# Performance work log

Hardware: AMD Instinct MI355X
Metric: run time of the kernel (lower is better)

The kernel has to match this reference:

```python
import jax, jax.numpy as jnp
import numpy as np


def _sdpa(q, k, v):
    # q: [B,H,Sq,D], k/v: [B,H,Sk,D]; torch F.scaled_dot_product_attention default scale
    scale = 1.0 / np.sqrt(q.shape[-1]).astype(np.float32)
    logits = jnp.einsum('bhqd,bhkd->bhqk', q, k) * scale
    w = jax.nn.softmax(logits, axis=-1)
    return jnp.einsum('bhqk,bhkd->bhqd', w, v)


def setup_inputs() -> dict:
    key = jax.random.key(0)
    ks = jax.random.split(key, 8)
    B2, S, C = 4, 1024, 1280  # full batch = [noise; ref], SDXL-like 32x32 latent
    Bh = B2 // 2
    w_init = 1.0 / np.sqrt(C).astype(np.float32)
    return {
        'hidden_states': jax.random.normal(ks[0], (B2, S, C), jnp.float32),
        'mask_ref': jax.random.uniform(ks[1], (Bh, S, 1), jnp.float32),
        'Wq': jax.random.normal(ks[2], (C, C), jnp.float32) * w_init,
        'Wk': jax.random.normal(ks[3], (C, C), jnp.float32) * w_init,
        'Wv': jax.random.normal(ks[4], (C, C), jnp.float32) * w_init,
        'Wo': jax.random.normal(ks[5], (C, C), jnp.float32) * w_init,
        'bo': jnp.zeros((C,), jnp.float32),
        'heads': 20,
    }


def reference(hidden_states, mask_ref, Wq, Wk, Wv, Wo, bo, heads):
    module_scale = 1.0  # self.scale
    B2, S, C = hidden_states.shape
    B = B2 // 2
    H = heads
    D = C // H
    noise = hidden_states[:B]
    ref = hidden_states[B:]

    # NOTE: faithful to source quirk: query uses the FULL 2B batch, then is
    # viewed as (B, 2S, H, D) -> q has query length 2S.
    query = jnp.einsum('bsc,oc->bso', hidden_states, Wq)  # [2B,S,C]
    q = query.reshape(B, 2 * S, H, D).transpose(0, 2, 1, 3)  # [B,H,2S,D]

    # background branch: self-attention over noise tokens
    k_bg = jnp.einsum('bsc,oc->bso', noise, Wk).reshape(B, S, H, D).transpose(0, 2, 1, 3)
    v_bg = jnp.einsum('bsc,oc->bso', noise, Wv).reshape(B, S, H, D).transpose(0, 2, 1, 3)
    hidden_bg = _sdpa(q, k_bg, v_bg).transpose(0, 2, 1, 3).reshape(B, 2 * S, C)

    # face branch: cross-attention onto reference tokens, K/V gated by mask_ref
    gate = mask_ref.reshape(B, 1, S, 1)  # [B,1,Sk,1]
    k_face = jnp.einsum('bsc,oc->bso', ref, Wk).reshape(B, S, H, D).transpose(0, 2, 1, 3) * gate
    v_face = jnp.einsum('bsc,oc->bso', ref, Wv).reshape(B, S, H, D).transpose(0, 2, 1, 3) * gate
    hidden_face = _sdpa(q, k_face, v_face).transpose(0, 2, 1, 3).reshape(B, 2 * S, C)

    merged = hidden_bg + hidden_face * module_scale  # mask is None -> additive merge
    out = jnp.einsum('bsc,oc->bso', merged, Wo) + bo  # to_out[0]; dropout is identity
    return out
```

## Files before the change

kernel.cpp:

```cpp
#include <hip/hip_runtime.h>
#include <hip/hip_bf16.h>

typedef __bf16 bf16;
typedef __bf16 bf16x8 __attribute__((ext_vector_type(8)));
typedef __bf16 bf16x4 __attribute__((ext_vector_type(4)));
typedef float f32x4 __attribute__((ext_vector_type(4)));

#define CDIM 1280

static __device__ __forceinline__ f32x4 mfma16(bf16x8 a, bf16x8 b, f32x4 c) {
  return __builtin_amdgcn_mfma_f32_16x16x32_bf16(a, b, c, 0, 0, 0);
}

static __device__ __forceinline__ void gload_lds(const bf16* g, bf16* l) {
  __builtin_amdgcn_global_load_lds(
      (const __attribute__((address_space(1))) void*)g,
      (__attribute__((address_space(3))) void*)l, 16, 0, 0);
}

static __device__ __forceinline__ float fexp2(float x) {
#if __has_builtin(__builtin_amdgcn_exp2f)
  return __builtin_amdgcn_exp2f(x);
#else
  return __expf(x * 0.6931471805599453f);
#endif
}

__global__ __launch_bounds__(256) void cvt_all(const float* __restrict__ h,
                                               const float* __restrict__ wq,
                                               const float* __restrict__ wk,
                                               const float* __restrict__ wv,
                                               const float* __restrict__ wo,
                                               bf16* __restrict__ hb, bf16* __restrict__ wqb,
                                               bf16* __restrict__ wkb, bf16* __restrict__ wvb,
                                               bf16* __restrict__ wob) {
  int id = blockIdx.x * 256 + threadIdx.x;
  const float* src; bf16* dst; int off;
  if (id < 1310720) { src = h; dst = hb; off = id; }
  else {
    int t = id - 1310720;
    int w = t / 409600; off = t % 409600;
    src = (w == 0) ? wq : (w == 1) ? wk : (w == 2) ? wv : wo;
    dst = (w == 0) ? wqb : (w == 1) ? wkb : (w == 2) ? wvb : wob;
  }
  float4 v = reinterpret_cast<const float4*>(src)[off];
  bf16x4 o;
  o[0] = (bf16)v.x; o[1] = (bf16)v.y; o[2] = (bf16)v.z; o[3] = (bf16)v.w;
  reinterpret_cast<bf16x4*>(dst)[off] = o;
}

__global__ __launch_bounds__(256) void qkv_gemm(const bf16* __restrict__ X,
                                                const bf16* __restrict__ Wq,
                                                const bf16* __restrict__ Wk,
                                                const bf16* __restrict__ Wv,
                                                const float* __restrict__ mask,
                                                bf16* __restrict__ Qb,
                                                bf16* __restrict__ Kb,
                                                bf16* __restrict__ Vt) {
  __shared__ bf16 Al[128 * 64];
  __shared__ bf16 Bl[128 * 64];
  const int tid = threadIdx.x, lane = tid & 63, wv = tid >> 6;
  const int lr = lane & 15, lg = lane >> 4;
  const int xb = blockIdx.x, by = blockIdx.y;
  const int wsel = xb / 10;
  const int cb = (xb % 10) * 128;
  const bf16* W = (wsel == 0) ? Wq : (wsel == 1) ? Wk : Wv;
  const int strow = tid >> 3, stchk = tid & 7;
  f32x4 acc[4][4] = {};
  for (int kt = 0; kt < 20; ++kt) {
    __syncthreads();
#pragma unroll
    for (int i = 0; i < 4; ++i) {
      gload_lds(X + (size_t)(by * 128 + i * 32 + strow) * CDIM + kt * 64 + stchk * 8,
                &Al[(i * 256 + tid) * 8]);
      gload_lds(W + (size_t)(cb + i * 32 + strow) * CDIM + kt * 64 + stchk * 8,
                &Bl[(i * 256 + tid) * 8]);
    }
    __syncthreads();
#pragma unroll
    for (int kk = 0; kk < 2; ++kk) {
      bf16x8 a[4], b[4];
#pragma unroll
      for (int i = 0; i < 4; ++i) {
        a[i] = *(const bf16x8*)&Al[((wv >> 1) * 64 + i * 16 + lr) * 64 + kk * 32 + lg * 8];
        b[i] = *(const bf16x8*)&Bl[((wv & 1) * 64 + i * 16 + lr) * 64 + kk * 32 + lg * 8];
      }
#pragma unroll
      for (int i = 0; i < 4; ++i)
#pragma unroll
        for (int j = 0; j < 4; ++j)
          acc[i][j] = mfma16(a[i], b[j], acc[i][j]);
    }
  }
  const int rbase = by * 128 + (wv >> 1) * 64;
  const int cbase = cb + (wv & 1) * 64;
  if (wsel == 2) {
#pragma unroll
    for (int i = 0; i < 4; ++i)
#pragma unroll
      for (int r = 0; r < 4; ++r) {
        const int row = rbase + i * 16 + lg * 4 + r;
        const float g = (row >= 2048) ? mask[row - 2048] : 1.0f;
        const int br = row >> 11, bb = (row >> 10) & 1, key = row & 1023;
#pragma unroll
        for (int j = 0; j < 4; ++j) {
          const int col = cbase + j * 16 + lr;
          const int hh = col >> 6, d = col & 63;
          Vt[(size_t)(br * 40 + bb * 20 + hh) * 65536 + d * 1024 + key] =
              (bf16)(acc[i][j][r] * g);
        }
      }
  } else {
    bf16* Y = (wsel == 0) ? Qb : Kb;
    const bool gated = (wsel == 1);
#pragma unroll
    for (int i = 0; i < 4; ++i)
#pragma unroll
      for (int r = 0; r < 4; ++r) {
        const int row = rbase + i * 16 + lg * 4 + r;
        const float g = (gated && row >= 2048) ? mask[row - 2048] : 1.0f;
#pragma unroll
        for (int j = 0; j < 4; ++j)
          Y[(size_t)row * CDIM + cbase + j * 16 + lr] = (bf16)(acc[i][j][r] * g);
      }
  }
}

__global__ __launch_bounds__(256) void attn_kernel(const bf16* __restrict__ Q,
                                                   const bf16* __restrict__ K,
                                                   const bf16* __restrict__ Vt,
                                                   bf16* __restrict__ Mg) {
  __shared__ bf16 Kl[2][64 * 64];
  __shared__ bf16 Vl[2][64 * 64];
  __shared__ bf16 Pl[4 * 16 * 64];
  const int tid = threadIdx.x, lane = tid & 63, wv = tid >> 6;
  const int lr = lane & 15, lg = lane >> 4;
  const int bid = blockIdx.x;
  const int sb = (bid & 7) * 160 + (bid >> 3);
  const int qt = sb & 31, hh = (sb >> 5) % 20, b = sb / 640;
  const int qrow = b * 2048 + qt * 64 + wv * 16;
  const int strow = tid >> 3, stchk = tid & 7;

  const bf16* Kb0 = K + (size_t)(b * 1024) * CDIM + hh * 64;
  const bf16* Vb0 = Vt + (size_t)(b * 20 + hh) * 65536;

  bf16x8 qf0, qf1;
  {
    const float SL2E = 0.125f * 1.4426950408889634f;
    const bf16* qp = Q + (size_t)(qrow + lr) * CDIM + hh * 64 + lg * 8;
    bf16x8 r0 = *(const bf16x8*)qp;
    bf16x8 r1 = *(const bf16x8*)(qp + 32);
#pragma unroll
    for (int j = 0; j < 8; ++j) {
      qf0[j] = (bf16)((float)r0[j] * SL2E);
      qf1[j] = (bf16)((float)r1[j] * SL2E);
    }
  }

  auto stage = [&](int t, int buf) {
    const int br = t >> 4, kt = t & 15;
    const bf16* Kp = Kb0 + (size_t)br * 2048 * CDIM;
    const bf16* Vp = Vb0 + (size_t)br * 40 * 65536;
#pragma unroll
    for (int i = 0; i < 2; ++i) {
      const int row = i * 32 + strow;
      gload_lds(Kp + (size_t)(kt * 64 + row) * CDIM + (stchk ^ (row & 7)) * 8,
                &Kl[buf][(i * 256 + tid) * 8]);
      gload_lds(Vp + (size_t)row * 1024 + kt * 64 + (stchk ^ (row & 7)) * 8,
                &Vl[buf][(i * 256 + tid) * 8]);
    }
  };

  float m = -INFINITY, l = 0.f;
  f32x4 O[4] = {};
  f32x4 Ofin[4] = {};

  stage(0, 0);
  __syncthreads();

  for (int t = 0; t < 32; ++t) {
    const int cur = t & 1;
    if (t < 31) stage(t + 1, cur ^ 1);

    f32x4 st4[4];
#pragma unroll
    for (int kb = 0; kb < 4; ++kb) {
      const int row = kb * 16 + lr;
      bf16x8 k0 = *(const bf16x8*)&Kl[cur][row * 64 + ((lg) ^ (lr & 7)) * 8];
      bf16x8 k1 = *(const bf16x8*)&Kl[cur][row * 64 + ((4 + lg) ^ (lr & 7)) * 8];
      f32x4 z = {};
      z = mfma16(k0, qf0, z);
      z = mfma16(k1, qf1, z);
      st4[kb] = z;
    }

    float pm = -INFINITY;
#pragma unroll
    for (int kb = 0; kb < 4; ++kb)
#pragma unroll
      for (int r = 0; r < 4; ++r) pm = fmaxf(pm, st4[kb][r]);
    pm = fmaxf(pm, __shfl_xor(pm, 16, 64));
    pm = fmaxf(pm, __shfl_xor(pm, 32, 64));

    float p[16], rs = 0.f;
    if (__all(pm <= m + 8.f)) {
#pragma unroll
      for (int kb = 0; kb < 4; ++kb)
#pragma unroll
        for (int r = 0; r < 4; ++r) {
          float e = fexp2(st4[kb][r] - m);
          p[kb * 4 + r] = e; rs += e;
        }
      rs += __shfl_xor(rs, 16, 64);
      rs += __shfl_xor(rs, 32, 64);
      l += rs;
    } else {
      const float mn = fmaxf(m, pm);
      const float al = fexp2(m - mn);
#pragma unroll
      for (int kb = 0; kb < 4; ++kb)
#pragma unroll
        for (int r = 0; r < 4; ++r) {
          float e = fexp2(st4[kb][r] - mn);
          p[kb * 4 + r] = e; rs += e;
        }
      rs += __shfl_xor(rs, 16, 64);
      rs += __shfl_xor(rs, 32, 64);
      l = l * al + rs;
      m = mn;
      float alr[4];
#pragma unroll
      for (int r = 0; r < 4; ++r) alr[r] = __shfl(al, lg * 4 + r, 64);
#pragma unroll
      for (int dt = 0; dt < 4; ++dt) {
        O[dt][0] *= alr[0]; O[dt][1] *= alr[1];
        O[dt][2] *= alr[2]; O[dt][3] *= alr[3];
      }
    }

#pragma unroll
    for (int kb = 0; kb < 4; ++kb) {
      const int chunk = (kb * 2 + (lg >> 1)) ^ (lr & 7);
      const int base = wv * 1024 + lr * 64 + chunk * 8 + (lg & 1) * 4;
      bf16x4 pk;
      pk[0] = (bf16)p[kb * 4 + 0]; pk[1] = (bf16)p[kb * 4 + 1];
      pk[2] = (bf16)p[kb * 4 + 2]; pk[3] = (bf16)p[kb * 4 + 3];
      *(bf16x4*)&Pl[base] = pk;
    }

    bf16x8 pa0 = *(const bf16x8*)&Pl[wv * 1024 + lr * 64 + ((lg) ^ (lr & 7)) * 8];
    bf16x8 pa1 = *(const bf16x8*)&Pl[wv * 1024 + lr * 64 + ((4 + lg) ^ (lr & 7)) * 8];
#pragma unroll
    for (int dt = 0; dt < 4; ++dt) {
      const int row = dt * 16 + lr;
      bf16x8 v0 = *(const bf16x8*)&Vl[cur][row * 64 + ((lg) ^ (lr & 7)) * 8];
      bf16x8 v1 = *(const bf16x8*)&Vl[cur][row * 64 + ((4 + lg) ^ (lr & 7)) * 8];
      O[dt] = mfma16(pa0, v0, O[dt]);
      O[dt] = mfma16(pa1, v1, O[dt]);
    }

    if (t == 15 || t == 31) {
      const float invl = 1.0f / l;
      float ivr[4];
#pragma unroll
      for (int r = 0; r < 4; ++r) ivr[r] = __shfl(invl, lg * 4 + r, 64);
#pragma unroll
      for (int dt = 0; dt < 4; ++dt) {
        Ofin[dt][0] += O[dt][0] * ivr[0]; Ofin[dt][1] += O[dt][1] * ivr[1];
        Ofin[dt][2] += O[dt][2] * ivr[2]; Ofin[dt][3] += O[dt][3] * ivr[3];
      }
      if (t == 15) {
        m = -INFINITY; l = 0.f;
#pragma unroll
        for (int dt = 0; dt < 4; ++dt) O[dt] = f32x4{};
      }
    }
    __syncthreads();
  }

#pragma unroll
  for (int dt = 0; dt < 4; ++dt)
#pragma unroll
    for (int r = 0; r < 4; ++r)
      Mg[(size_t)(qrow + lg * 4 + r) * CDIM + hh * 64 + dt * 16 + lr] = (bf16)Ofin[dt][r];
}

__global__ __launch_bounds__(256) void out_gemm(const bf16* __restrict__ X,
                                                const bf16* __restrict__ W,
                                                const float* __restrict__ bias,
                                                float* __restrict__ Y) {
  __shared__ bf16 Al[128 * 64];
  __shared__ bf16 Bl[128 * 64];
  const int tid = threadIdx.x, lane = tid & 63, wv = tid >> 6;
  const int lr = lane & 15, lg = lane >> 4;
  const int cb = blockIdx.x * 128, by = blockIdx.y;
  const int strow = tid >> 3, stchk = tid & 7;
  f32x4 acc[4][4] = {};
  for (int kt = 0; kt < 20; ++kt) {
    __syncthreads();
#pragma unroll
    for (int i = 0; i < 4; ++i) {
      gload_lds(X + (size_t)(by * 128 + i * 32 + strow) * CDIM + kt * 64 + stchk * 8,
                &Al[(i * 256 + tid) * 8]);
      gload_lds(W + (size_t)(cb + i * 32 + strow) * CDIM + kt * 64 + stchk * 8,
                &Bl[(i * 256 + tid) * 8]);
    }
    __syncthreads();
#pragma unroll
    for (int kk = 0; kk < 2; ++kk) {
      bf16x8 a[4], b[4];
#pragma unroll
      for (int i = 0; i < 4; ++i) {
        a[i] = *(const bf16x8*)&Al[((wv >> 1) * 64 + i * 16 + lr) * 64 + kk * 32 + lg * 8];
        b[i] = *(const bf16x8*)&Bl[((wv & 1) * 64 + i * 16 + lr) * 64 + kk * 32 + lg * 8];
      }
#pragma unroll
      for (int i = 0; i < 4; ++i)
#pragma unroll
        for (int j = 0; j < 4; ++j)
          acc[i][j] = mfma16(a[i], b[j], acc[i][j]);
    }
  }
  const int rbase = by * 128 + (wv >> 1) * 64;
  const int cbase = cb + (wv & 1) * 64;
#pragma unroll
  for (int i = 0; i < 4; ++i)
#pragma unroll
    for (int r = 0; r < 4; ++r) {
      const int row = rbase + i * 16 + lg * 4 + r;
#pragma unroll
      for (int j = 0; j < 4; ++j) {
        const int col = cbase + j * 16 + lr;
        Y[(size_t)row * CDIM + col] = acc[i][j][r] + bias[col];
      }
    }
}

extern "C" void kernel_launch(void* const* d_in, const int* in_sizes, int n_in,
                              void* d_out, int out_size, void* d_ws, size_t ws_size,
                              hipStream_t stream) {
  const float* hidden = (const float*)d_in[0];
  const float* mask   = (const float*)d_in[1];
  const float* Wq     = (const float*)d_in[2];
  const float* Wk     = (const float*)d_in[3];
  const float* Wv     = (const float*)d_in[4];
  const float* Wo     = (const float*)d_in[5];
  const float* bo     = (const float*)d_in[6];
  float* out = (float*)d_out;

  char* ws = (char*)d_ws;
  bf16* hb  = (bf16*)(ws);
  bf16* wqb = (bf16*)(ws + 10485760);
  bf16* wkb = (bf16*)(ws + 13762560);
  bf16* wvb = (bf16*)(ws + 17039360);
  bf16* wob = (bf16*)(ws + 20316160);
  bf16* Qb  = (bf16*)(ws + 23592960);
  bf16* Kb  = (bf16*)(ws + 34078720);
  bf16* Vt  = (bf16*)(ws + 44564480);
  bf16* Mg  = hb;

  cvt_all<<<dim3(11520), 256, 0, stream>>>(hidden, Wq, Wk, Wv, Wo, hb, wqb, wkb, wvb, wob);
  qkv_gemm<<<dim3(30, 32), 256, 0, stream>>>(hb, wqb, wkb, wvb, mask, Qb, Kb, Vt);
  attn_kernel<<<dim3(1280), 256, 0, stream>>>(Qb, Kb, Vt, Mg);
  out_gemm<<<dim3(10, 32), 256, 0, stream>>>(Mg, wob, bo, out);
}
```

Before: 226.1 us.

## Keep attention probabilities in registers by computing transposed PV product

Drops the LDS round-trip for the softmax probability tile. The PV MMA is swapped so V supplies the A operand and P stays in registers as the B operand, which yields O transposed. Rows then map to lanes directly, so the per-row alpha and 1/l shuffles go away and the output store becomes a vectorized 4-wide write. It also raises wave priority around the MFMA sections with s_setprio, at the cost of narrower 4-element LDS reads for V.

```diff
diff --git a/kernel.cpp b/kernel.cpp
--- a/kernel.cpp
+++ b/kernel.cpp
@@ -132,7 +132,6 @@
                                                    bf16* __restrict__ Mg) {
   __shared__ bf16 Kl[2][64 * 64];
   __shared__ bf16 Vl[2][64 * 64];
-  __shared__ bf16 Pl[4 * 16 * 64];
   const int tid = threadIdx.x, lane = tid & 63, wv = tid >> 6;
   const int lr = lane & 15, lg = lane >> 4;
   const int bid = blockIdx.x;
@@ -174,6 +173,7 @@
   float m = -INFINITY, l = 0.f;
   f32x4 O[4] = {};
   f32x4 Ofin[4] = {};
+  const int sw = lr & 7;
 
   stage(0, 0);
   __syncthreads();
@@ -183,16 +183,18 @@
     if (t < 31) stage(t + 1, cur ^ 1);
 
     f32x4 st4[4];
+    __builtin_amdgcn_s_setprio(1);
 #pragma unroll
     for (int kb = 0; kb < 4; ++kb) {
       const int row = kb * 16 + lr;
-      bf16x8 k0 = *(const bf16x8*)&Kl[cur][row * 64 + ((lg) ^ (lr & 7)) * 8];
-      bf16x8 k1 = *(const bf16x8*)&Kl[cur][row * 64 + ((4 + lg) ^ (lr & 7)) * 8];
+      bf16x8 k0 = *(const bf16x8*)&Kl[cur][row * 64 + (lg ^ sw) * 8];
+      bf16x8 k1 = *(const bf16x8*)&Kl[cur][row * 64 + ((4 + lg) ^ sw) * 8];
       f32x4 z = {};
       z = mfma16(k0, qf0, z);
       z = mfma16(k1, qf1, z);
       st4[kb] = z;
     }
+    __builtin_amdgcn_s_setprio(0);
 
     float pm = -INFINITY;
 #pragma unroll
@@ -228,46 +230,37 @@
       rs += __shfl_xor(rs, 32, 64);
       l = l * al + rs;
       m = mn;
-      float alr[4];
-#pragma unroll
-      for (int r = 0; r < 4; ++r) alr[r] = __shfl(al, lg * 4 + r, 64);
 #pragma unroll
       for (int dt = 0; dt < 4; ++dt) {
-        O[dt][0] *= alr[0]; O[dt][1] *= alr[1];
-        O[dt][2] *= alr[2]; O[dt][3] *= alr[3];
-      }
-    }
-
-#pragma unroll
-    for (int kb = 0; kb < 4; ++kb) {
-      const int chunk = (kb * 2 + (lg >> 1)) ^ (lr & 7);
-      const int base = wv * 1024 + lr * 64 + chunk * 8 + (lg & 1) * 4;
-      bf16x4 pk;
-      pk[0] = (bf16)p[kb * 4 + 0]; pk[1] = (bf16)p[kb * 4 + 1];
-      pk[2] = (bf16)p[kb * 4 + 2]; pk[3] = (bf16)p[kb * 4 + 3];
-      *(bf16x4*)&Pl[base] = pk;
-    }
-
-    bf16x8 pa0 = *(const bf16x8*)&Pl[wv * 1024 + lr * 64 + ((lg) ^ (lr & 7)) * 8];
-    bf16x8 pa1 = *(const bf16x8*)&Pl[wv * 1024 + lr * 64 + ((4 + lg) ^ (lr & 7)) * 8];
+        O[dt][0] *= al; O[dt][1] *= al; O[dt][2] *= al; O[dt][3] *= al;
+      }
+    }
+
+    bf16x8 pb0, pb1;
+#pragma unroll
+    for (int e = 0; e < 8; ++e) { pb0[e] = (bf16)p[e]; pb1[e] = (bf16)p[8 + e]; }
+
+    __builtin_amdgcn_s_setprio(1);
 #pragma unroll
     for (int dt = 0; dt < 4; ++dt) {
-      const int row = dt * 16 + lr;
-      bf16x8 v0 = *(const bf16x8*)&Vl[cur][row * 64 + ((lg) ^ (lr & 7)) * 8];
-      bf16x8 v1 = *(const bf16x8*)&Vl[cur][row * 64 + ((4 + lg) ^ (lr & 7)) * 8];
-      O[dt] = mfma16(pa0, v0, O[dt]);
-      O[dt] = mfma16(pa1, v1, O[dt]);
-    }
+      const int rowb = (dt * 16 + lr) * 64;
+      bf16x4 a0 = *(const bf16x4*)&Vl[cur][rowb + (((lg >> 1)) ^ sw) * 8 + (lg & 1) * 4];
+      bf16x4 a1 = *(const bf16x4*)&Vl[cur][rowb + ((2 + (lg >> 1)) ^ sw) * 8 + (lg & 1) * 4];
+      bf16x4 a2 = *(const bf16x4*)&Vl[cur][rowb + ((4 + (lg >> 1)) ^ sw) * 8 + (lg & 1) * 4];
+      bf16x4 a3 = *(const bf16x4*)&Vl[cur][rowb + ((6 + (lg >> 1)) ^ sw) * 8 + (lg & 1) * 4];
+      bf16x8 A0 = {a0[0], a0[1], a0[2], a0[3], a1[0], a1[1], a1[2], a1[3]};
+      bf16x8 A1 = {a2[0], a2[1], a2[2], a2[3], a3[0], a3[1], a3[2], a3[3]};
+      O[dt] = mfma16(A0, pb0, O[dt]);
+      O[dt] = mfma16(A1, pb1, O[dt]);
+    }
+    __builtin_amdgcn_s_setprio(0);
 
     if (t == 15 || t == 31) {
       const float invl = 1.0f / l;
-      float ivr[4];
-#pragma unroll
-      for (int r = 0; r < 4; ++r) ivr[r] = __shfl(invl, lg * 4 + r, 64);
 #pragma unroll
       for (int dt = 0; dt < 4; ++dt) {
-        Ofin[dt][0] += O[dt][0] * ivr[0]; Ofin[dt][1] += O[dt][1] * ivr[1];
-        Ofin[dt][2] += O[dt][2] * ivr[2]; Ofin[dt][3] += O[dt][3] * ivr[3];
+        Ofin[dt][0] += O[dt][0] * invl; Ofin[dt][1] += O[dt][1] * invl;
+        Ofin[dt][2] += O[dt][2] * invl; Ofin[dt][3] += O[dt][3] * invl;
       }
       if (t == 15) {
         m = -INFINITY; l = 0.f;
@@ -279,10 +272,12 @@
   }
 
 #pragma unroll
-  for (int dt = 0; dt < 4; ++dt)
-#pragma unroll
-    for (int r = 0; r < 4; ++r)
-      Mg[(size_t)(qrow + lg * 4 + r) * CDIM + hh * 64 + dt * 16 + lr] = (bf16)Ofin[dt][r];
+  for (int dt = 0; dt < 4; ++dt) {
+    bf16x4 o4;
+    o4[0] = (bf16)Ofin[dt][0]; o4[1] = (bf16)Ofin[dt][1];
+    o4[2] = (bf16)Ofin[dt][2]; o4[3] = (bf16)Ofin[dt][3];
+    *(bf16x4*)&Mg[(size_t)(qrow + lr) * CDIM + hh * 64 + dt * 16 + lg * 4] = o4;
+  }
 }
 
 __global__ __launch_bounds__(256) void out_gemm(const bf16* __restrict__ X,
```

Result: slower. 232.1 us (+2.6%).
